# Performance work log

Measured on AMD Instinct MI355X. Metric: run time of the kernel, lower is better.

The kernel has to match this reference:

```python
import jax, jax.numpy as jnp
import numpy as np

BLOCK = 32           # sparsity_config.block
STRIDE_BLOCKS = 4    # stride 128 // block 32
B, H, L, HD = 2, 16, 4096, 64


def _make_fixed_layout(nb, bs):
    """DeepSpeed 'fixed' unidirectional layout, numverts=vertsize=1 (same for all heads)."""
    lay = np.zeros((nb, nb), dtype=np.int64)
    # local: lower-triangular within each stride window
    for i in range(0, nb, bs):
        for j in range(i, i + bs):
            lay[j, i:j + 1] = 1
    # global: vertical stripe at column offset bs-1 of every window, causal (col < row)
    start = bs - 1
    for i in range(nb):
        for j in range(start, i, bs):
            lay[i, j] = 1
    rows, cols = np.nonzero(lay)  # sorted by row
    return jnp.asarray(rows, jnp.int32), jnp.asarray(cols, jnp.int32)


def setup_inputs() -> dict:
    key = jax.random.key(0)
    kq, kk, kv = jax.random.split(key, 3)
    query = jax.random.normal(kq, (B, H, L, HD), jnp.float32)
    key_t = jax.random.normal(kk, (B, H, L, HD), jnp.float32)
    value = jax.random.normal(kv, (B, H, L, HD), jnp.float32)
    rows, cols = _make_fixed_layout(L // BLOCK, STRIDE_BLOCKS)
    return {"query": query, "key": key_t, "value": value,
            "rows": rows, "cols": cols, "block": BLOCK}


def reference(query, key, value, rows, cols, block):
    b, h, l, hd = query.shape
    nb = l // block
    scale = float(hd) ** (-0.5)
    # [nb, B, H, block, hd] with block-row axis leading for gather/scatter
    qb = jnp.moveaxis(query.reshape(b, h, nb, block, hd), 2, 0)
    kb = jnp.moveaxis(key.reshape(b, h, nb, block, hd), 2, 0)
    vb = jnp.moveaxis(value.reshape(b, h, nb, block, hd), 2, 0)
    # sdd: scores only on active blocks -> [nnz, B, H, block, block]
    s = jnp.einsum('nbhqd,nbhkd->nbhqk', qb[rows], kb[cols]) * scale
    # block-sparse softmax over each query row (segment reduce over blocks sharing a row)
    m_blk = s.max(-1)  # [nnz, B, H, block]
    row_max = jnp.full((nb, b, h, block), -jnp.inf, s.dtype).at[rows].max(m_blk)
    e = jnp.exp(s - row_max[rows][..., None])
    denom = jnp.zeros((nb, b, h, block), s.dtype).at[rows].add(e.sum(-1))
    p = e / denom[rows][..., None]
    # dsd: probs @ value, scatter-add into block rows
    ob = jnp.zeros((nb, b, h, block, hd), s.dtype).at[rows].add(
        jnp.einsum('nbhqk,nbhkd->nbhqd', p, vb[cols]))
    return jnp.moveaxis(ob, 0, 2).reshape(b, h, l, hd)
```

## Files before the change

kernel.cpp:

```cpp
#include <hip/hip_runtime.h>
#include <math.h>

#define BH    32
#define LSEQ  4096
#define HD    64
#define BLK   32
#define NB    128
#define NWIN  32
#define QSCALE 0.18033688011112042f

#define KSTR 34
#define VSTR 17

typedef _Float16 h2  __attribute__((ext_vector_type(2)));
typedef _Float16 h8  __attribute__((ext_vector_type(8)));
typedef float    f16v __attribute__((ext_vector_type(16)));

static __device__ __forceinline__ h2 pk(float a, float b) {
    return __builtin_bit_cast(h2, __builtin_amdgcn_cvt_pkrtz(a, b));
}
static __device__ __forceinline__ unsigned pku(float a, float b) {
    return __builtin_bit_cast(unsigned, __builtin_amdgcn_cvt_pkrtz(a, b));
}
static __device__ __forceinline__ short h16(float x) {
    return __builtin_bit_cast(short, (_Float16)x);
}
static __device__ __forceinline__ h8 mk8(h2 a, h2 b, h2 c, h2 d) {
    h8 r;
    r[0] = a[0]; r[1] = a[1]; r[2] = b[0]; r[3] = b[1];
    r[4] = c[0]; r[5] = c[1]; r[6] = d[0]; r[7] = d[1];
    return r;
}

__global__ __launch_bounds__(256)
void sparse_attn_win4(const float* __restrict__ Q, const float* __restrict__ K,
                      const float* __restrict__ V, float* __restrict__ out)
{
    const int id = (int)blockIdx.x;
    const int cc = id & 255;
    const int k  = id >> 8;
    const int v  = cc & 31;
    const int u  = cc >> 5;
    const int bh = u + 8 * k;
    int w;
    switch (k) {
        case 0:  w = v;              break;
        case 1:  w = (47 - v) & 31;  break;
        case 2:  w = (v + 16) & 31;  break;
        default: w = (63 - v) & 31;  break;
    }

    const int t    = (int)threadIdx.x;
    const int d    = t >> 6;
    const int lane = t & 63;
    const int l31  = lane & 31;
    const int h    = lane >> 5;
    const int r    = 4 * w + d;

    __shared__ __align__(16) unsigned kbuf[2][BLK * KSTR];
    __shared__ __align__(16) unsigned vbuf[2][HD * VSTR];

    const size_t base = (size_t)bh * (LSEQ * HD);

    const float* qp = Q + base + (size_t)(r * BLK + l31) * HD + 8 * h;
    h8 qf[4];
#pragma unroll
    for (int tt = 0; tt < 4; ++tt) {
        float4 a = *(const float4*)(qp + 16 * tt);
        float4 b = *(const float4*)(qp + 16 * tt + 4);
        qf[tt] = mk8(pk(a.x * QSCALE, a.y * QSCALE), pk(a.z * QSCALE, a.w * QSCALE),
                     pk(b.x * QSCALE, b.y * QSCALE), pk(b.z * QSCALE, b.w * QSCALE));
    }

    f16v o0 = {}, o1 = {};
    float2 ls2 = make_float2(0.0f, 0.0f);

    const int n    = w + 4;
    const int srow = t >> 3;
    const int sdg  = t & 7;

    const float* kgb = K + base + (size_t)srow * HD + sdg * 8;
    const float* vgb = V + base + (size_t)srow * HD + sdg * 8;

    float4 kA, kB, vA, vB;

    auto colOf = [&](int j) { return (j < w) ? (4 * j + 3) : (4 * w + (j - w)); };

    auto loadR = [&](int j) {
        const size_t off = (size_t)colOf(j) * (BLK * HD);
        kA = *(const float4*)(kgb + off);
        kB = *(const float4*)(kgb + off + 4);
        vA = *(const float4*)(vgb + off);
        vB = *(const float4*)(vgb + off + 4);
    };
    auto writeL = [&](int b) {
        uint2 w0, w1;
        w0.x = pku(kA.x, kA.y); w0.y = pku(kA.z, kA.w);
        w1.x = pku(kB.x, kB.y); w1.y = pku(kB.z, kB.w);
        *(uint2*)&kbuf[b][srow * KSTR + sdg * 4]     = w0;
        *(uint2*)&kbuf[b][srow * KSTR + sdg * 4 + 2] = w1;
        short* vs = (short*)&vbuf[b][0];
        const int vd0 = sdg * 8;
        vs[(vd0 + 0) * (2 * VSTR) + srow] = h16(vA.x);
        vs[(vd0 + 1) * (2 * VSTR) + srow] = h16(vA.y);
        vs[(vd0 + 2) * (2 * VSTR) + srow] = h16(vA.z);
        vs[(vd0 + 3) * (2 * VSTR) + srow] = h16(vA.w);
        vs[(vd0 + 4) * (2 * VSTR) + srow] = h16(vB.x);
        vs[(vd0 + 5) * (2 * VSTR) + srow] = h16(vB.y);
        vs[(vd0 + 6) * (2 * VSTR) + srow] = h16(vB.z);
        vs[(vd0 + 7) * (2 * VSTR) + srow] = h16(vB.w);
    };

    loadR(0);

    for (int j = 0; j < n; ++j) {
        writeL(j & 1);
        if (j + 1 < n) loadR(j + 1);
        __builtin_amdgcn_s_waitcnt(0xc07f);
        __builtin_amdgcn_s_barrier();

        if (j < w || (j - w) <= d) {
            const unsigned* kb = kbuf[j & 1];
            const unsigned* vb = vbuf[j & 1];

            f16v st = {};
#pragma unroll
            for (int tt = 0; tt < 4; ++tt) {
                const int kw = l31 * KSTR + 8 * tt + 4 * h;
                uint2 u0 = *(const uint2*)&kb[kw];
                uint2 u1 = *(const uint2*)&kb[kw + 2];
                uint4 uu; uu.x = u0.x; uu.y = u0.y; uu.z = u1.x; uu.w = u1.y;
                h8 kf = __builtin_bit_cast(h8, uu);
                st = __builtin_amdgcn_mfma_f32_32x32x16_f16(kf, qf[tt], st, 0, 0, 0);
            }

            float ps[16];
#pragma unroll
            for (int g = 0; g < 16; ++g) ps[g] = __builtin_exp2f(st[g]);
#pragma unroll
            for (int g = 0; g < 8; ++g) {
                ls2.x += ps[2 * g];
                ls2.y += ps[2 * g + 1];
            }
            h2 ph[8];
#pragma unroll
            for (int jj = 0; jj < 8; ++jj) ph[jj] = pk(ps[2 * jj], ps[2 * jj + 1]);

#pragma unroll
            for (int t2 = 0; t2 < 2; ++t2) {
                h2 s0 = h ? ph[4 * t2]     : ph[4 * t2 + 2];
                h2 s1 = h ? ph[4 * t2 + 1] : ph[4 * t2 + 3];
                int i0 = __shfl_xor(__builtin_bit_cast(int, s0), 32);
                int i1 = __shfl_xor(__builtin_bit_cast(int, s1), 32);
                h2 g0 = __builtin_bit_cast(h2, i0), g1 = __builtin_bit_cast(h2, i1);
                h2 c0 = h ? g0 : ph[4 * t2];
                h2 c1 = h ? g1 : ph[4 * t2 + 1];
                h2 c2 = h ? ph[4 * t2 + 2] : g0;
                h2 c3 = h ? ph[4 * t2 + 3] : g1;
                h8 pa = mk8(c0, c1, c2, c3);

                const int va0 = l31 * VSTR + 8 * t2 + 4 * h;
                const int va1 = (32 + l31) * VSTR + 8 * t2 + 4 * h;
                uint4 u0, u1;
                u0.x = vb[va0]; u0.y = vb[va0 + 1]; u0.z = vb[va0 + 2]; u0.w = vb[va0 + 3];
                u1.x = vb[va1]; u1.y = vb[va1 + 1]; u1.z = vb[va1 + 2]; u1.w = vb[va1 + 3];
                h8 vf0 = __builtin_bit_cast(h8, u0);
                h8 vf1 = __builtin_bit_cast(h8, u1);
                o0 = __builtin_amdgcn_mfma_f32_32x32x16_f16(pa, vf0, o0, 0, 0, 0);
                o1 = __builtin_amdgcn_mfma_f32_32x32x16_f16(pa, vf1, o1, 0, 0, 0);
            }
        }
    }

    float lsum = ls2.x + ls2.y;
    lsum += __shfl_xor(lsum, 32);
    const float inv = 1.0f / lsum;

    float* op = out + base + (size_t)(r * BLK) * HD;
#pragma unroll
    for (int g = 0; g < 16; ++g) {
        const int qrow = (g & 3) + 8 * (g >> 2) + 4 * h;
        int iv = __builtin_amdgcn_ds_bpermute(qrow << 2, __float_as_int(inv));
        const float invq = __int_as_float(iv);
        op[(size_t)qrow * HD + l31]      = o0[g] * invq;
        op[(size_t)qrow * HD + 32 + l31] = o1[g] * invq;
    }
}

extern "C" void kernel_launch(void* const* d_in, const int* in_sizes, int n_in,
                              void* d_out, int out_size, void* d_ws, size_t ws_size,
                              hipStream_t stream) {
    const float* Q = (const float*)d_in[0];
    const float* K = (const float*)d_in[1];
    const float* V = (const float*)d_in[2];

    dim3 grid(NWIN * BH);
    dim3 block(256);
    sparse_attn_win4<<<grid, block, 0, stream>>>(Q, K, V, (float*)d_out);
}
```

Measured before the change: 170.1 us.

## Pair short and long windows per block to balance causal work

```diff
diff --git a/kernel.cpp b/kernel.cpp
--- a/kernel.cpp
+++ b/kernel.cpp
@@ -33,49 +33,24 @@
 }
 
 __global__ __launch_bounds__(256)
-void sparse_attn_win4(const float* __restrict__ Q, const float* __restrict__ K,
+void sparse_attn_pair(const float* __restrict__ Q, const float* __restrict__ K,
                       const float* __restrict__ V, float* __restrict__ out)
 {
     const int id = (int)blockIdx.x;
-    const int cc = id & 255;
-    const int k  = id >> 8;
-    const int v  = cc & 31;
-    const int u  = cc >> 5;
-    const int bh = u + 8 * k;
-    int w;
-    switch (k) {
-        case 0:  w = v;              break;
-        case 1:  w = (47 - v) & 31;  break;
-        case 2:  w = (v + 16) & 31;  break;
-        default: w = (63 - v) & 31;  break;
-    }
+    const int bh = id & 31;
+    const int p  = id >> 5;
 
     const int t    = (int)threadIdx.x;
     const int d    = t >> 6;
     const int lane = t & 63;
     const int l31  = lane & 31;
     const int h    = lane >> 5;
-    const int r    = 4 * w + d;
 
     __shared__ __align__(16) unsigned kbuf[2][BLK * KSTR];
     __shared__ __align__(16) unsigned vbuf[2][HD * VSTR];
 
     const size_t base = (size_t)bh * (LSEQ * HD);
 
-    const float* qp = Q + base + (size_t)(r * BLK + l31) * HD + 8 * h;
-    h8 qf[4];
-#pragma unroll
-    for (int tt = 0; tt < 4; ++tt) {
-        float4 a = *(const float4*)(qp + 16 * tt);
-        float4 b = *(const float4*)(qp + 16 * tt + 4);
-        qf[tt] = mk8(pk(a.x * QSCALE, a.y * QSCALE), pk(a.z * QSCALE, a.w * QSCALE),
-                     pk(b.x * QSCALE, b.y * QSCALE), pk(b.z * QSCALE, b.w * QSCALE));
-    }
-
-    f16v o0 = {}, o1 = {};
-    float2 ls2 = make_float2(0.0f, 0.0f);
-
-    const int n    = w + 4;
     const int srow = t >> 3;
     const int sdg  = t & 7;
 
@@ -84,10 +59,9 @@
 
     float4 kA, kB, vA, vB;
 
-    auto colOf = [&](int j) { return (j < w) ? (4 * j + 3) : (4 * w + (j - w)); };
-
-    auto loadR = [&](int j) {
-        const size_t off = (size_t)colOf(j) * (BLK * HD);
+    auto loadR = [&](int w, int j) {
+        const int col = (j < w) ? (4 * j + 3) : (4 * w + (j - w));
+        const size_t off = (size_t)col * (BLK * HD);
         kA = *(const float4*)(kgb + off);
         kB = *(const float4*)(kgb + off + 4);
         vA = *(const float4*)(vgb + off);
@@ -111,79 +85,100 @@
         vs[(vd0 + 7) * (2 * VSTR) + srow] = h16(vB.w);
     };
 
-    loadR(0);
+    int pb = 0;
+    loadR(p, 0);
 
-    for (int j = 0; j < n; ++j) {
-        writeL(j & 1);
-        if (j + 1 < n) loadR(j + 1);
-        __builtin_amdgcn_s_waitcnt(0xc07f);
-        __builtin_amdgcn_s_barrier();
+    for (int ph = 0; ph < 2; ++ph) {
+        const int w = ph ? (31 - p) : p;
+        const int r = 4 * w + d;
+        const int n = w + 4;
 
-        if (j < w || (j - w) <= d) {
-            const unsigned* kb = kbuf[j & 1];
-            const unsigned* vb = vbuf[j & 1];
+        const float* qp = Q + base + (size_t)(r * BLK + l31) * HD + 8 * h;
+        h8 qf[4];
+#pragma unroll
+        for (int tt = 0; tt < 4; ++tt) {
+            float4 a = *(const float4*)(qp + 16 * tt);
+            float4 b = *(const float4*)(qp + 16 * tt + 4);
+            qf[tt] = mk8(pk(a.x * QSCALE, a.y * QSCALE), pk(a.z * QSCALE, a.w * QSCALE),
+                         pk(b.x * QSCALE, b.y * QSCALE), pk(b.z * QSCALE, b.w * QSCALE));
+        }
 
-            f16v st = {};
+        f16v o0 = {}, o1 = {};
+        float2 ls2 = make_float2(0.0f, 0.0f);
+
+        for (int j = 0; j < n; ++j, pb ^= 1) {
+            writeL(pb);
+            if (j + 1 < n)      loadR(w, j + 1);
+            else if (ph == 0)   loadR(31 - p, 0);
+            __builtin_amdgcn_s_waitcnt(0xc07f);
+            __builtin_amdgcn_s_barrier();
+
+            if (j < w || (j - w) <= d) {
+                const unsigned* kb = kbuf[pb];
+                const unsigned* vb = vbuf[pb];
+
+                f16v st = {};
 #pragma unroll
-            for (int tt = 0; tt < 4; ++tt) {
-                const int kw = l31 * KSTR + 8 * tt + 4 * h;
-                uint2 u0 = *(const uint2*)&kb[kw];
-                uint2 u1 = *(const uint2*)&kb[kw + 2];
-                uint4 uu; uu.x = u0.x; uu.y = u0.y; uu.z = u1.x; uu.w = u1.y;
-                h8 kf = __builtin_bit_cast(h8, uu);
-                st = __builtin_amdgcn_mfma_f32_32x32x16_f16(kf, qf[tt], st, 0, 0, 0);
-            }
+                for (int tt = 0; tt < 4; ++tt) {
+                    const int kw = l31 * KSTR + 8 * tt + 4 * h;
+                    uint2 u0 = *(const uint2*)&kb[kw];
+                    uint2 u1 = *(const uint2*)&kb[kw + 2];
+                    uint4 uu; uu.x = u0.x; uu.y = u0.y; uu.z = u1.x; uu.w = u1.y;
+                    h8 kf = __builtin_bit_cast(h8, uu);
+                    st = __builtin_amdgcn_mfma_f32_32x32x16_f16(kf, qf[tt], st, 0, 0, 0);
+                }
 
-            float ps[16];
+                float ps[16];
 #pragma unroll
-            for (int g = 0; g < 16; ++g) ps[g] = __builtin_exp2f(st[g]);
+                for (int g = 0; g < 16; ++g) ps[g] = __builtin_exp2f(st[g]);
 #pragma unroll
-            for (int g = 0; g < 8; ++g) {
-                ls2.x += ps[2 * g];
-                ls2.y += ps[2 * g + 1];
-            }
-            h2 ph[8];
+                for (int g = 0; g < 8; ++g) {
+                    ls2.x += ps[2 * g];
+                    ls2.y += ps[2 * g + 1];
+                }
+                h2 ph2[8];
 #pragma unroll
-            for (int jj = 0; jj < 8; ++jj) ph[jj] = pk(ps[2 * jj], ps[2 * jj + 1]);
+                for (int jj = 0; jj < 8; ++jj) ph2[jj] = pk(ps[2 * jj], ps[2 * jj + 1]);
 
 #pragma unroll
-            for (int t2 = 0; t2 < 2; ++t2) {
-                h2 s0 = h ? ph[4 * t2]     : ph[4 * t2 + 2];
-                h2 s1 = h ? ph[4 * t2 + 1] : ph[4 * t2 + 3];
-                int i0 = __shfl_xor(__builtin_bit_cast(int, s0), 32);
-                int i1 = __shfl_xor(__builtin_bit_cast(int, s1), 32);
-                h2 g0 = __builtin_bit_cast(h2, i0), g1 = __builtin_bit_cast(h2, i1);
-                h2 c0 = h ? g0 : ph[4 * t2];
-                h2 c1 = h ? g1 : ph[4 * t2 + 1];
-                h2 c2 = h ? ph[4 * t2 + 2] : g0;
-                h2 c3 = h ? ph[4 * t2 + 3] : g1;
-                h8 pa = mk8(c0, c1, c2, c3);
+                for (int t2 = 0; t2 < 2; ++t2) {
+                    h2 s0 = h ? ph2[4 * t2]     : ph2[4 * t2 + 2];
+                    h2 s1 = h ? ph2[4 * t2 + 1] : ph2[4 * t2 + 3];
+                    int i0 = __shfl_xor(__builtin_bit_cast(int, s0), 32);
+                    int i1 = __shfl_xor(__builtin_bit_cast(int, s1), 32);
+                    h2 g0 = __builtin_bit_cast(h2, i0), g1 = __builtin_bit_cast(h2, i1);
+                    h2 c0 = h ? g0 : ph2[4 * t2];
+                    h2 c1 = h ? g1 : ph2[4 * t2 + 1];
+                    h2 c2 = h ? ph2[4 * t2 + 2] : g0;
+                    h2 c3 = h ? ph2[4 * t2 + 3] : g1;
+                    h8 pa = mk8(c0, c1, c2, c3);
 
-                const int va0 = l31 * VSTR + 8 * t2 + 4 * h;
-                const int va1 = (32 + l31) * VSTR + 8 * t2 + 4 * h;
-                uint4 u0, u1;
-                u0.x = vb[va0]; u0.y = vb[va0 + 1]; u0.z = vb[va0 + 2]; u0.w = vb[va0 + 3];
-                u1.x = vb[va1]; u1.y = vb[va1 + 1]; u1.z = vb[va1 + 2]; u1.w = vb[va1 + 3];
-                h8 vf0 = __builtin_bit_cast(h8, u0);
-                h8 vf1 = __builtin_bit_cast(h8, u1);
-                o0 = __builtin_amdgcn_mfma_f32_32x32x16_f16(pa, vf0, o0, 0, 0, 0);
-                o1 = __builtin_amdgcn_mfma_f32_32x32x16_f16(pa, vf1, o1, 0, 0, 0);
+                    const int va0 = l31 * VSTR + 8 * t2 + 4 * h;
+                    const int va1 = (32 + l31) * VSTR + 8 * t2 + 4 * h;
+                    uint4 u0, u1;
+                    u0.x = vb[va0]; u0.y = vb[va0 + 1]; u0.z = vb[va0 + 2]; u0.w = vb[va0 + 3];
+                    u1.x = vb[va1]; u1.y = vb[va1 + 1]; u1.z = vb[va1 + 2]; u1.w = vb[va1 + 3];
+                    h8 vf0 = __builtin_bit_cast(h8, u0);
+                    h8 vf1 = __builtin_bit_cast(h8, u1);
+                    o0 = __builtin_amdgcn_mfma_f32_32x32x16_f16(pa, vf0, o0, 0, 0, 0);
+                    o1 = __builtin_amdgcn_mfma_f32_32x32x16_f16(pa, vf1, o1, 0, 0, 0);
+                }
             }
         }
-    }
 
-    float lsum = ls2.x + ls2.y;
-    lsum += __shfl_xor(lsum, 32);
-    const float inv = 1.0f / lsum;
+        float lsum = ls2.x + ls2.y;
+        lsum += __shfl_xor(lsum, 32);
+        const float inv = 1.0f / lsum;
 
-    float* op = out + base + (size_t)(r * BLK) * HD;
+        float* op = out + base + (size_t)(r * BLK) * HD;
 #pragma unroll
-    for (int g = 0; g < 16; ++g) {
-        const int qrow = (g & 3) + 8 * (g >> 2) + 4 * h;
-        int iv = __builtin_amdgcn_ds_bpermute(qrow << 2, __float_as_int(inv));
-        const float invq = __int_as_float(iv);
-        op[(size_t)qrow * HD + l31]      = o0[g] * invq;
-        op[(size_t)qrow * HD + 32 + l31] = o1[g] * invq;
+        for (int g = 0; g < 16; ++g) {
+            const int qrow = (g & 3) + 8 * (g >> 2) + 4 * h;
+            int iv = __builtin_amdgcn_ds_bpermute(qrow << 2, __float_as_int(inv));
+            const float invq = __int_as_float(iv);
+            op[(size_t)qrow * HD + l31]      = o0[g] * invq;
+            op[(size_t)qrow * HD + 32 + l31] = o1[g] * invq;
+        }
     }
 }
 
@@ -194,7 +189,7 @@
     const float* K = (const float*)d_in[1];
     const float* V = (const float*)d_in[2];
 
-    dim3 grid(NWIN * BH);
+    dim3 grid(NWIN * BH / 2);
     dim3 block(256);
-    sparse_attn_win4<<<grid, block, 0, stream>>>(Q, K, V, (float*)d_out);
+    sparse_attn_pair<<<grid, block, 0, stream>>>(Q, K, V, (float*)d_out);
 }
```

New measurement: 165.5 us. 2.7% less time.
